# Performance work log

Hardware: AMD Instinct MI355X
Metric: run time of the kernel (lower is better)

The kernel has to match this reference:

```python
import jax, jax.numpy as jnp
import numpy as np

N, E, F, S = 20000, 160000, 16, 8
ECC1, ECC2, ECC3 = 40, 24, 24
DS = [96, 256, 768, 512, 64, 1]


def setup_inputs() -> dict:
    key = jax.random.key(0)
    ks = iter(jax.random.split(key, 40))
    inp = {}
    inp["x"] = jax.random.normal(next(ks), (N, F), dtype=jnp.float32)
    inp["edge_index"] = jax.random.randint(next(ks), (E, 2), 0, N, dtype=jnp.int32)
    inp["e"] = jax.random.uniform(next(ks), (E, S), dtype=jnp.float32)

    def dense_p(k, fi, fo):
        return (jax.random.normal(k, (fi, fo), dtype=jnp.float32) * (1.0 / np.sqrt(fi)),
                jnp.zeros((fo,), dtype=jnp.float32))

    # ECCConv params: kernel_network dense (S -> F_in*F_out), root kernel, bias
    for i, (fi, fo) in enumerate([(F, ECC1), (ECC1, ECC2), (ECC2, ECC3)], start=1):
        We, be = dense_p(next(ks), S, fi * fo)
        root, _ = dense_p(next(ks), fi, fo)
        inp[f"We{i}"], inp[f"be{i}"] = We, be
        inp[f"root{i}"], inp[f"b{i}"] = root, jnp.zeros((fo,), dtype=jnp.float32)

    dims = [ECC3] + DS
    for i in range(6):
        W, b = dense_p(next(ks), dims[i], dims[i + 1])
        inp[f"Wd{i+1}"], inp[f"bd{i+1}"] = W, b
    return inp


def _ecc(h, src, tgt, e, We, be, root, b):
    fi, fo = root.shape
    # per-edge filter matrices from edge features: [E, F_in, F_out]
    K = (e @ We + be).reshape(e.shape[0], fi, fo)
    msg = jnp.einsum('ef,efo->eo', h[src], K)          # gather + per-edge matvec
    agg = jax.ops.segment_sum(msg, tgt, num_segments=h.shape[0])  # scatter-add
    return jax.nn.relu(agg + h @ root + b)


def reference(x, edge_index, e,
              We1, be1, root1, b1,
              We2, be2, root2, b2,
              We3, be3, root3, b3,
              Wd1, bd1, Wd2, bd2, Wd3, bd3, Wd4, bd4, Wd5, bd5, Wd6, bd6):
    src, tgt = edge_index[:, 0], edge_index[:, 1]
    h = _ecc(x, src, tgt, e, We1, be1, root1, b1)
    h = _ecc(h, src, tgt, e, We2, be2, root2, b2)
    h = _ecc(h, src, tgt, e, We3, be3, root3, b3)
    g = jnp.sum(h, axis=0, keepdims=True)  # GlobalSumPool (single mode) -> [1, 24]
    for W, b in [(Wd1, bd1), (Wd2, bd2), (Wd3, bd3), (Wd4, bd4), (Wd5, bd5)]:
        g = jax.nn.relu(g @ W + b)
    return g @ Wd6 + bd6  # [1, 1]
```

## Files before the change

kernel.cpp:

```cpp
#include <hip/hip_runtime.h>

constexpr int NN  = 20000;
constexpr int NE  = 160000;
constexpr int CAP = 32;
constexpr int TN  = 32;
constexpr int NBM = 16;

__device__ inline void gstore(float* p, float v) {
    __hip_atomic_store(p, v, __ATOMIC_RELAXED, __HIP_MEMORY_SCOPE_AGENT);
}
__device__ inline float gload(const float* p) {
    return __hip_atomic_load(p, __ATOMIC_RELAXED, __HIP_MEMORY_SCOPE_AGENT);
}

__device__ inline void mbarrier(int* ctr, int target, bool wait) {
    __syncthreads();
    if (threadIdx.x == 0) {
        __threadfence();
        __hip_atomic_fetch_add(ctr, 1, __ATOMIC_ACQ_REL, __HIP_MEMORY_SCOPE_AGENT);
        if (wait)
            while (__hip_atomic_load(ctr, __ATOMIC_ACQUIRE, __HIP_MEMORY_SCOPE_AGENT) < target) {}
    }
    __syncthreads();
}

template<int FI, int FO2>
__device__ void stage_W(float* Wlds, const float* __restrict__ We,
                        const float* __restrict__ be, const float* __restrict__ root)
{
    constexpr int PW = 10 * FO2, C4 = PW / 4, O4 = FO2 / 4;
    for (int t = threadIdx.x; t < FI * C4; t += 256) {
        const int f = t / C4, r = t % C4, s = r / O4, oq = r % O4;
        const float4* src;
        if (s < 8)       src = (const float4*)(We + (size_t)s * FI * FO2 + f * FO2 + oq * 4);
        else if (s == 8) src = (const float4*)(be + f * FO2 + oq * 4);
        else             src = (const float4*)(root + f * FO2 + oq * 4);
        ((float4*)Wlds)[t] = *src;
    }
}

template<int FI, int FO2>
__device__ void gemm_tile(const float* htile, const float* Wlds,
                          const float* __restrict__ bias, float* __restrict__ Pout, int n0)
{
    constexpr int PW = 10 * FO2, C4 = PW / 4, O4 = FO2 / 4;
    constexpr int TPN = 256 / TN;
    const int nl = threadIdx.x / TPN;
    const int lane = threadIdx.x % TPN;
    const int n = n0 + nl;
    if (n >= NN) return;
    const float*  hr = &htile[nl * (FI + 4)];
    const float4* W4 = (const float4*)Wlds;
    float4* Pr = (float4*)(Pout + (size_t)n * PW);
    for (int cc = lane; cc < C4; cc += TPN) {
        float4 a = {0.f, 0.f, 0.f, 0.f};
        #pragma unroll
        for (int f = 0; f < FI; f++) {
            const float  hf = hr[f];
            const float4 w  = W4[f * C4 + cc];
            a.x = fmaf(hf, w.x, a.x); a.y = fmaf(hf, w.y, a.y);
            a.z = fmaf(hf, w.z, a.z); a.w = fmaf(hf, w.w, a.w);
        }
        if (cc >= 9 * O4) {
            const float4 b4 = ((const float4*)bias)[cc - 9 * O4];
            a.x += b4.x; a.y += b4.y; a.z += b4.z; a.w += b4.w;
        }
        Pr[cc] = a;
    }
}

__global__ __launch_bounds__(256)
void fill_nodeP1_kernel(const int* __restrict__ eidx, const float* __restrict__ x,
                        const float* __restrict__ We1, const float* __restrict__ be1,
                        const float* __restrict__ root1, const float* __restrict__ b1,
                        int* __restrict__ cnt_s, int* __restrict__ cnt_t,
                        int* __restrict__ se_eid, int* __restrict__ te_slot,
                        float* __restrict__ Pa)
{
    __shared__ float smem[16 * 400 + TN * 20];
    const int b = blockIdx.x, tid = threadIdx.x;
    if (b < 625) {
        const int eid = b * 256 + tid;
        const int2 st = ((const int2*)eidx)[eid];
        const int qs = atomicAdd(&cnt_s[st.x], 1);
        if (qs < CAP) {
            se_eid[st.x * CAP + qs] = eid;
            const int qt = atomicAdd(&cnt_t[st.y], 1);
            if (qt < CAP) te_slot[st.y * CAP + qt] = st.x * CAP + qs;
        }
    } else {
        float* Wlds  = smem;
        float* htile = smem + 6400;
        stage_W<16, 40>(Wlds, We1, be1, root1);
        const int n0 = (b - 625) * TN;
        for (int t = tid; t < TN * 4; t += 256) {
            const int nl = t / 4, fq = t % 4;
            const int n = n0 + nl;
            float4 v = {0.f, 0.f, 0.f, 0.f};
            if (n < NN) v = ((const float4*)(x + (size_t)n * 16))[fq];
            *((float4*)&htile[nl * 20 + fq * 4]) = v;
        }
        __syncthreads();
        gemm_tile<16, 40>(htile, Wlds, b1, Pa, n0);
    }
}

template<int FO, int PW1, int GSZ>
__global__ __launch_bounds__(256)
void push_msg_kernel(const float* __restrict__ Pin, const int* __restrict__ cnt_s,
                     const int* __restrict__ se_eid, const float* __restrict__ e,
                     float* __restrict__ msg)
{
    constexpr int SPB = 256 / GSZ;
    const int tid = threadIdx.x;
    const int o   = tid % GSZ;
    const int n   = blockIdx.x * SPB + tid / GSZ;

    float p[9];
    if (o < FO) {
        #pragma unroll
        for (int s = 0; s < 9; s++)
            p[s] = Pin[(size_t)n * PW1 + s * FO + o];
    }
    const int d = min(cnt_s[n], CAP);
    const int* eb = se_eid + n * CAP;
    float* mb = msg + (size_t)n * CAP * FO;
    #pragma unroll 2
    for (int j = 0; j < d; j++) {
        const int eid = eb[j];
        const float4 e0 = *(const float4*)(e + (size_t)eid * 8);
        const float4 e1 = *(const float4*)(e + (size_t)eid * 8 + 4);
        if (o < FO) {
            float m = p[8];
            m = fmaf(e0.x, p[0], m); m = fmaf(e0.y, p[1], m);
            m = fmaf(e0.z, p[2], m); m = fmaf(e0.w, p[3], m);
            m = fmaf(e1.x, p[4], m); m = fmaf(e1.y, p[5], m);
            m = fmaf(e1.z, p[6], m); m = fmaf(e1.w, p[7], m);
            mb[j * FO + o] = m;
        }
    }
}

template<int FI, int FO2>
__global__ __launch_bounds__(256)
void msg_gemm_kernel(const float* __restrict__ msg, const int* __restrict__ cnt_t,
                     const int* __restrict__ te_slot, const float* __restrict__ Pin,
                     const float* __restrict__ We, const float* __restrict__ be,
                     const float* __restrict__ root, const float* __restrict__ bias,
                     float* __restrict__ Pout)
{
    constexpr int PW_IN = 10 * FI, HS = FI + 4, OQ = FI / 4;
    __shared__ float smem[FI * 10 * FO2 + TN * HS];
    float* Wlds  = smem;
    float* htile = smem + FI * 10 * FO2;
    stage_W<FI, FO2>(Wlds, We, be, root);
    const int n0 = blockIdx.x * TN;
    for (int t = threadIdx.x; t < TN * OQ; t += 256) {
        const int nl = t / OQ, oq = t % OQ;
        const int n = n0 + nl;
        float4 acc = *(const float4*)(Pin + (size_t)n * PW_IN + 9 * FI + oq * 4);
        const int d = min(cnt_t[n], CAP);
        const int* tb = te_slot + n * CAP;
        #pragma unroll 2
        for (int k = 0; k < d; k++) {
            const int slot = tb[k];
            const float4 v = *(const float4*)(msg + (size_t)slot * FI + oq * 4);
            acc.x += v.x; acc.y += v.y; acc.z += v.z; acc.w += v.w;
        }
        float4 r = {fmaxf(acc.x, 0.f), fmaxf(acc.y, 0.f),
                    fmaxf(acc.z, 0.f), fmaxf(acc.w, 0.f)};
        *(float4*)&htile[nl * HS + oq * 4] = r;
    }
    __syncthreads();
    gemm_tile<FI, FO2>(htile, Wlds, bias, Pout, n0);
}

__global__ __launch_bounds__(256)
void msg_colsum_kernel(const float* __restrict__ msg, const int* __restrict__ cnt_t,
                       const int* __restrict__ te_slot, const float* __restrict__ Pin,
                       float* __restrict__ g)
{
    constexpr int FO = 24, OQ = 6;
    __shared__ float gl[FO];
    const int tid = threadIdx.x;
    if (tid < FO) gl[tid] = 0.f;
    __syncthreads();
    for (int i = blockIdx.x * 256 + tid; i < NN * OQ; i += gridDim.x * 256) {
        const int n = i / OQ, oq = i - n * OQ;
        float4 acc = *(const float4*)(Pin + (size_t)n * 240 + 216 + oq * 4);
        const int d = min(cnt_t[n], CAP);
        const int* tb = te_slot + n * CAP;
        #pragma unroll 2
        for (int k = 0; k < d; k++) {
            const int slot = tb[k];
            const float4 v = *(const float4*)(msg + (size_t)slot * FO + oq * 4);
            acc.x += v.x; acc.y += v.y; acc.z += v.z; acc.w += v.w;
        }
        atomicAdd(&gl[oq * 4 + 0], fmaxf(acc.x, 0.f));
        atomicAdd(&gl[oq * 4 + 1], fmaxf(acc.y, 0.f));
        atomicAdd(&gl[oq * 4 + 2], fmaxf(acc.z, 0.f));
        atomicAdd(&gl[oq * 4 + 3], fmaxf(acc.w, 0.f));
    }
    __syncthreads();
    if (tid < FO) unsafeAtomicAdd(&g[tid], gl[tid]);
}

__global__ __launch_bounds__(256)
void mlp_kernel(const float* __restrict__ g, int* __restrict__ ctr,
                const float* __restrict__ Wd1, const float* __restrict__ bd1,
                const float* __restrict__ Wd2, const float* __restrict__ bd2,
                const float* __restrict__ Wd3, const float* __restrict__ bd3,
                const float* __restrict__ Wd4, const float* __restrict__ bd4,
                const float* __restrict__ Wd5, const float* __restrict__ bd5,
                const float* __restrict__ Wd6, const float* __restrict__ bd6,
                float* __restrict__ m3, float* __restrict__ m4,
                float* __restrict__ out)
{
    __shared__ float v0[768];
    __shared__ float v1[96];
    __shared__ float red[256];
    const int tid = threadIdx.x, b = blockIdx.x;

    if (tid < 24) v0[tid] = g[tid];
    __syncthreads();
    if (tid < 96) {
        float a = bd1[tid];
        #pragma unroll
        for (int i = 0; i < 24; i++) a = fmaf(v0[i], Wd1[i * 96 + tid], a);
        v1[tid] = fmaxf(a, 0.f);
    }
    __syncthreads();

    {
        float a = bd2[tid];
        #pragma unroll
        for (int i = 0; i < 96; i++) a = fmaf(v1[i], Wd2[i * 256 + tid], a);
        red[tid] = fmaxf(a, 0.f);
    }
    __syncthreads();
    v0[tid] = red[tid];
    __syncthreads();

    if (tid < 192) {
        const int o = b * 48 + (tid % 48), kg = tid / 48;
        float a = 0.f;
        #pragma unroll 8
        for (int i = kg * 64; i < kg * 64 + 64; i++)
            a = fmaf(v0[i], Wd3[(size_t)i * 768 + o], a);
        red[tid] = a;
    }
    __syncthreads();
    if (tid < 48) {
        float s = bd3[b * 48 + tid] + red[tid] + red[48 + tid] + red[96 + tid] + red[144 + tid];
        gstore(&m3[b * 48 + tid], fmaxf(s, 0.f));
    }
    mbarrier(ctr, 1 * NBM, true);

    for (int i = tid; i < 768; i += 256) v0[i] = gload(&m3[i]);
    __syncthreads();
    {
        const int o = b * 32 + (tid & 31), kg = tid >> 5;
        float a = 0.f;
        #pragma unroll 8
        for (int i = kg * 96; i < kg * 96 + 96; i++)
            a = fmaf(v0[i], Wd4[(size_t)i * 512 + o], a);
        red[tid] = a;
    }
    __syncthreads();
    if (tid < 32) {
        float s = bd4[b * 32 + tid];
        #pragma unroll
        for (int k = 0; k < 8; k++) s += red[k * 32 + tid];
        gstore(&m4[b * 32 + tid], fmaxf(s, 0.f));
    }
    mbarrier(ctr, 2 * NBM, b == 0);

    if (b == 0) {
        for (int i = tid; i < 512; i += 256) v0[i] = gload(&m4[i]);
        __syncthreads();
        {
            const int o = tid & 63, kg = tid >> 6;
            float a = 0.f;
            #pragma unroll 8
            for (int i = kg * 128; i < kg * 128 + 128; i++)
                a = fmaf(v0[i], Wd5[(size_t)i * 64 + o], a);
            red[tid] = a;
        }
        __syncthreads();
        if (tid < 64) {
            float s = bd5[tid] + red[tid] + red[64 + tid] + red[128 + tid] + red[192 + tid];
            float v = fmaxf(s, 0.f) * Wd6[tid];
            #pragma unroll
            for (int off = 32; off > 0; off >>= 1)
                v += __shfl_down(v, off, 64);
            if (tid == 0) out[0] = v + bd6[0];
        }
    }
}

extern "C" void kernel_launch(void* const* d_in, const int* in_sizes, int n_in,
                              void* d_out, int out_size, void* d_ws, size_t ws_size,
                              hipStream_t stream)
{
    const float* x     = (const float*)d_in[0];
    const int*   eidx  = (const int*)  d_in[1];
    const float* e     = (const float*)d_in[2];
    const float* We1   = (const float*)d_in[3];  const float* be1 = (const float*)d_in[4];
    const float* root1 = (const float*)d_in[5];  const float* b1  = (const float*)d_in[6];
    const float* We2   = (const float*)d_in[7];  const float* be2 = (const float*)d_in[8];
    const float* root2 = (const float*)d_in[9];  const float* b2  = (const float*)d_in[10];
    const float* We3   = (const float*)d_in[11]; const float* be3 = (const float*)d_in[12];
    const float* root3 = (const float*)d_in[13]; const float* b3  = (const float*)d_in[14];
    const float* Wd1 = (const float*)d_in[15]; const float* bd1 = (const float*)d_in[16];
    const float* Wd2 = (const float*)d_in[17]; const float* bd2 = (const float*)d_in[18];
    const float* Wd3 = (const float*)d_in[19]; const float* bd3 = (const float*)d_in[20];
    const float* Wd4 = (const float*)d_in[21]; const float* bd4 = (const float*)d_in[22];
    const float* Wd5 = (const float*)d_in[23]; const float* bd5 = (const float*)d_in[24];
    const float* Wd6 = (const float*)d_in[25]; const float* bd6 = (const float*)d_in[26];

    int*   wi      = (int*)d_ws;
    float* wf      = (float*)d_ws;
    int*   cnt_s   = wi;
    int*   cnt_t   = wi + 20000;
    float* g       = wf + 40000;
    int*   mctr    = wi + 40064;
    float* m3      = wf + 40096;
    float* m4      = m3 + 768;
    int*   se_eid  = wi + 41376;
    int*   te_slot = wi + 681376;
    float* Pa      = wf + 1321376;
    float* Pb      = wf + 9321376;
    float* msg     = wf + 14121376;

    hipMemsetAsync(d_ws, 0, (size_t)41376 * sizeof(float), stream);

    fill_nodeP1_kernel<<<1250, 256, 0, stream>>>(eidx, x, We1, be1, root1, b1,
                                                 cnt_s, cnt_t, se_eid, te_slot, Pa);

    push_msg_kernel<40, 400, 64><<<NN / 4, 256, 0, stream>>>(Pa, cnt_s, se_eid, e, msg);

    msg_gemm_kernel<40, 24><<<625, 256, 0, stream>>>(msg, cnt_t, te_slot, Pa,
                                                     We2, be2, root2, b2, Pb);

    push_msg_kernel<24, 240, 32><<<NN / 8, 256, 0, stream>>>(Pb, cnt_s, se_eid, e, msg);

    msg_gemm_kernel<24, 24><<<625, 256, 0, stream>>>(msg, cnt_t, te_slot, Pb,
                                                     We3, be3, root3, b3, Pa);

    push_msg_kernel<24, 240, 32><<<NN / 8, 256, 0, stream>>>(Pa, cnt_s, se_eid, e, msg);

    msg_colsum_kernel<<<512, 256, 0, stream>>>(msg, cnt_t, te_slot, Pa, g);

    mlp_kernel<<<NBM, 256, 0, stream>>>(g, mctr,
                                        Wd1, bd1, Wd2, bd2, Wd3, bd3,
                                        Wd4, bd4, Wd5, bd5, Wd6, bd6,
                                        m3, m4, (float*)d_out);
}
```

Before: 263.1 us.

## Fuse per-layer node GEMM with edge message push, keep P tile in LDS

Merges each layer's node GEMM with the following edge-message push kernel, so the per-node 9-segment projection stays in LDS and only the root/bias segment is written to global memory. Tiles shrink to 8 nodes per block, weights are staged in two halves to fit LDS, and the target-side gather is split across several threads per feature with LDS atomics. Bucketing moves into its own kernel. This removes the large global P round-trip and two launches, but it restages the full weight matrix in every one of 2500 blocks and adds more barriers.

Result: no change. 258.3 us (-1.8%).

```diff
diff --git a/kernel.cpp b/kernel.cpp
--- a/kernel.cpp
+++ b/kernel.cpp
@@ -3,7 +3,7 @@
 constexpr int NN  = 20000;
 constexpr int NE  = 160000;
 constexpr int CAP = 32;
-constexpr int TN  = 32;
+constexpr int TN2 = 8;
 constexpr int NBM = 16;
 
 __device__ inline void gstore(float* p, float v) {
@@ -24,160 +24,225 @@
     __syncthreads();
 }
 
-template<int FI, int FO2>
-__device__ void stage_W(float* Wlds, const float* __restrict__ We,
-                        const float* __restrict__ be, const float* __restrict__ root)
-{
-    constexpr int PW = 10 * FO2, C4 = PW / 4, O4 = FO2 / 4;
-    for (int t = threadIdx.x; t < FI * C4; t += 256) {
-        const int f = t / C4, r = t % C4, s = r / O4, oq = r % O4;
+template<int FI, int FO2, int CH>
+__device__ void stage_half(float* Wh, const float* __restrict__ We,
+                           const float* __restrict__ be, const float* __restrict__ root,
+                           int c0)
+{
+    constexpr int O4 = FO2 / 4;
+    for (int t = threadIdx.x; t < FI * CH; t += 256) {
+        const int f = t / CH, ccp = t % CH, cc = c0 + ccp;
+        const int s = cc / O4, oq = cc % O4;
         const float4* src;
         if (s < 8)       src = (const float4*)(We + (size_t)s * FI * FO2 + f * FO2 + oq * 4);
         else if (s == 8) src = (const float4*)(be + f * FO2 + oq * 4);
         else             src = (const float4*)(root + f * FO2 + oq * 4);
-        ((float4*)Wlds)[t] = *src;
+        ((float4*)Wh)[t] = *src;
     }
 }
 
 template<int FI, int FO2>
-__device__ void gemm_tile(const float* htile, const float* Wlds,
-                          const float* __restrict__ bias, float* __restrict__ Pout, int n0)
-{
-    constexpr int PW = 10 * FO2, C4 = PW / 4, O4 = FO2 / 4;
-    constexpr int TPN = 256 / TN;
-    const int nl = threadIdx.x / TPN;
-    const int lane = threadIdx.x % TPN;
-    const int n = n0 + nl;
-    if (n >= NN) return;
-    const float*  hr = &htile[nl * (FI + 4)];
-    const float4* W4 = (const float4*)Wlds;
-    float4* Pr = (float4*)(Pout + (size_t)n * PW);
-    for (int cc = lane; cc < C4; cc += TPN) {
+__device__ void gemm_half_PL(const float* htile, const float* Wh,
+                             const float* __restrict__ bias,
+                             float* P_lds, float* __restrict__ seg9g,
+                             int n0, int c0)
+{
+    constexpr int PW = 10 * FO2, C4 = PW / 4, CH = C4 / 2, O4 = FO2 / 4;
+    constexpr int PL = 9 * FO2;
+    constexpr int TPN = 256 / TN2;
+    constexpr int HS  = FI + 4;
+    const int nl = threadIdx.x / TPN, lane = threadIdx.x % TPN;
+    const float*  hr = &htile[nl * HS];
+    const float4* W4 = (const float4*)Wh;
+    for (int ccp = lane; ccp < CH; ccp += TPN) {
+        const int cc = c0 + ccp;
         float4 a = {0.f, 0.f, 0.f, 0.f};
         #pragma unroll
         for (int f = 0; f < FI; f++) {
             const float  hf = hr[f];
-            const float4 w  = W4[f * C4 + cc];
+            const float4 w  = W4[f * CH + ccp];
             a.x = fmaf(hf, w.x, a.x); a.y = fmaf(hf, w.y, a.y);
             a.z = fmaf(hf, w.z, a.z); a.w = fmaf(hf, w.w, a.w);
         }
-        if (cc >= 9 * O4) {
+        if (cc < 9 * O4) {
+            *(float4*)&P_lds[nl * PL + cc * 4] = a;
+        } else {
             const float4 b4 = ((const float4*)bias)[cc - 9 * O4];
             a.x += b4.x; a.y += b4.y; a.z += b4.z; a.w += b4.w;
-        }
-        Pr[cc] = a;
+            *(float4*)&seg9g[(size_t)(n0 + nl) * FO2 + (cc - 9 * O4) * 4] = a;
+        }
+    }
+}
+
+template<int FO2>
+__device__ void push_phase(const float* P_lds, const int* __restrict__ cnt_s,
+                           const int* __restrict__ se_eid, const float* __restrict__ e,
+                           float* __restrict__ msg, float* scratch, int n0)
+{
+    constexpr int PL = 9 * FO2, OQ2 = FO2 / 4;
+    float* elds = scratch;
+    int*   esl  = (int*)(scratch + 2048);
+    int*   enl  = esl + 256;
+    int*   offs = enl + 256;
+    const int tid = threadIdx.x;
+    if (tid == 0) {
+        int a = 0;
+        for (int i = 0; i < TN2; i++) { offs[i] = a; a += min(cnt_s[n0 + i], CAP); }
+        offs[TN2] = a;
+    }
+    __syncthreads();
+    const int ET = offs[TN2];
+    for (int T = tid; T < ET; T += 256) {
+        int nl = 0;
+        #pragma unroll
+        for (int i = 1; i < TN2; i++) nl += (T >= offs[i]);
+        const int j    = T - offs[nl];
+        const int slot = (n0 + nl) * CAP + j;
+        const int eid  = se_eid[slot];
+        esl[T] = slot; enl[T] = nl;
+        *(float4*)&elds[T * 8]     = *(const float4*)(e + (size_t)eid * 8);
+        *(float4*)&elds[T * 8 + 4] = *(const float4*)(e + (size_t)eid * 8 + 4);
+    }
+    __syncthreads();
+    for (int T = tid; T < ET * OQ2; T += 256) {
+        const int ed = T / OQ2, oq = T % OQ2;
+        const int nl = enl[ed], slot = esl[ed];
+        const float* Pr = &P_lds[nl * PL + oq * 4];
+        const float* ee = &elds[ed * 8];
+        float4 m = *(const float4*)(Pr + 8 * FO2);
+        #pragma unroll
+        for (int s = 0; s < 8; s++) {
+            const float  es = ee[s];
+            const float4 w  = *(const float4*)(Pr + s * FO2);
+            m.x = fmaf(es, w.x, m.x); m.y = fmaf(es, w.y, m.y);
+            m.z = fmaf(es, w.z, m.z); m.w = fmaf(es, w.w, m.w);
+        }
+        *(float4*)&msg[(size_t)slot * FO2 + oq * 4] = m;
     }
 }
 
 __global__ __launch_bounds__(256)
-void fill_nodeP1_kernel(const int* __restrict__ eidx, const float* __restrict__ x,
-                        const float* __restrict__ We1, const float* __restrict__ be1,
-                        const float* __restrict__ root1, const float* __restrict__ b1,
-                        int* __restrict__ cnt_s, int* __restrict__ cnt_t,
-                        int* __restrict__ se_eid, int* __restrict__ te_slot,
-                        float* __restrict__ Pa)
-{
-    __shared__ float smem[16 * 400 + TN * 20];
-    const int b = blockIdx.x, tid = threadIdx.x;
-    if (b < 625) {
-        const int eid = b * 256 + tid;
-        const int2 st = ((const int2*)eidx)[eid];
-        const int qs = atomicAdd(&cnt_s[st.x], 1);
-        if (qs < CAP) {
-            se_eid[st.x * CAP + qs] = eid;
-            const int qt = atomicAdd(&cnt_t[st.y], 1);
-            if (qt < CAP) te_slot[st.y * CAP + qt] = st.x * CAP + qs;
-        }
-    } else {
-        float* Wlds  = smem;
-        float* htile = smem + 6400;
-        stage_W<16, 40>(Wlds, We1, be1, root1);
-        const int n0 = (b - 625) * TN;
-        for (int t = tid; t < TN * 4; t += 256) {
-            const int nl = t / 4, fq = t % 4;
-            const int n = n0 + nl;
-            float4 v = {0.f, 0.f, 0.f, 0.f};
-            if (n < NN) v = ((const float4*)(x + (size_t)n * 16))[fq];
-            *((float4*)&htile[nl * 20 + fq * 4]) = v;
-        }
-        __syncthreads();
-        gemm_tile<16, 40>(htile, Wlds, b1, Pa, n0);
-    }
-}
-
-template<int FO, int PW1, int GSZ>
-__global__ __launch_bounds__(256)
-void push_msg_kernel(const float* __restrict__ Pin, const int* __restrict__ cnt_s,
-                     const int* __restrict__ se_eid, const float* __restrict__ e,
-                     float* __restrict__ msg)
-{
-    constexpr int SPB = 256 / GSZ;
+void bucket_kernel(const int* __restrict__ eidx,
+                   int* __restrict__ cnt_s, int* __restrict__ cnt_t,
+                   int* __restrict__ se_eid, int* __restrict__ te_slot)
+{
+    const int eid = blockIdx.x * 256 + threadIdx.x;
+    const int2 st = ((const int2*)eidx)[eid];
+    const int qs = atomicAdd(&cnt_s[st.x], 1);
+    if (qs < CAP) {
+        se_eid[st.x * CAP + qs] = eid;
+        const int qt = atomicAdd(&cnt_t[st.y], 1);
+        if (qt < CAP) te_slot[st.y * CAP + qt] = st.x * CAP + qs;
+    }
+}
+
+__global__ __launch_bounds__(256, 4)
+void l1_push_kernel(const float* __restrict__ x,
+                    const float* __restrict__ We1, const float* __restrict__ be1,
+                    const float* __restrict__ root1, const float* __restrict__ b1,
+                    const int* __restrict__ cnt_s, const int* __restrict__ se_eid,
+                    const float* __restrict__ e,
+                    float* __restrict__ seg9_1, float* __restrict__ msg1)
+{
+    constexpr int FI = 16, FO2 = 40, CH = 50;
+    constexpr int WHF = FI * CH * 4;
+    constexpr int PLF = TN2 * 9 * FO2;
+    constexpr int HTF = TN2 * (FI + 4);
+    __shared__ float smem[WHF + PLF + HTF];
+    float* Wh    = smem;
+    float* P_lds = smem + WHF;
+    float* htile = smem + WHF + PLF;
     const int tid = threadIdx.x;
-    const int o   = tid % GSZ;
-    const int n   = blockIdx.x * SPB + tid / GSZ;
-
-    float p[9];
-    if (o < FO) {
-        #pragma unroll
-        for (int s = 0; s < 9; s++)
-            p[s] = Pin[(size_t)n * PW1 + s * FO + o];
-    }
-    const int d = min(cnt_s[n], CAP);
-    const int* eb = se_eid + n * CAP;
-    float* mb = msg + (size_t)n * CAP * FO;
-    #pragma unroll 2
-    for (int j = 0; j < d; j++) {
-        const int eid = eb[j];
-        const float4 e0 = *(const float4*)(e + (size_t)eid * 8);
-        const float4 e1 = *(const float4*)(e + (size_t)eid * 8 + 4);
-        if (o < FO) {
-            float m = p[8];
-            m = fmaf(e0.x, p[0], m); m = fmaf(e0.y, p[1], m);
-            m = fmaf(e0.z, p[2], m); m = fmaf(e0.w, p[3], m);
-            m = fmaf(e1.x, p[4], m); m = fmaf(e1.y, p[5], m);
-            m = fmaf(e1.z, p[6], m); m = fmaf(e1.w, p[7], m);
-            mb[j * FO + o] = m;
-        }
-    }
-}
-
-template<int FI, int FO2>
-__global__ __launch_bounds__(256)
-void msg_gemm_kernel(const float* __restrict__ msg, const int* __restrict__ cnt_t,
-                     const int* __restrict__ te_slot, const float* __restrict__ Pin,
-                     const float* __restrict__ We, const float* __restrict__ be,
-                     const float* __restrict__ root, const float* __restrict__ bias,
-                     float* __restrict__ Pout)
-{
-    constexpr int PW_IN = 10 * FI, HS = FI + 4, OQ = FI / 4;
-    __shared__ float smem[FI * 10 * FO2 + TN * HS];
-    float* Wlds  = smem;
-    float* htile = smem + FI * 10 * FO2;
-    stage_W<FI, FO2>(Wlds, We, be, root);
-    const int n0 = blockIdx.x * TN;
-    for (int t = threadIdx.x; t < TN * OQ; t += 256) {
-        const int nl = t / OQ, oq = t % OQ;
+    const int n0  = blockIdx.x * TN2;
+
+    stage_half<FI, FO2, CH>(Wh, We1, be1, root1, 0);
+    for (int t = tid; t < TN2 * 4; t += 256) {
+        const int nl = t / 4, fq = t % 4;
+        *(float4*)&htile[nl * 20 + fq * 4] =
+            *(const float4*)(x + (size_t)(n0 + nl) * 16 + fq * 4);
+    }
+    __syncthreads();
+    gemm_half_PL<FI, FO2>(htile, Wh, b1, P_lds, seg9_1, n0, 0);
+    __syncthreads();
+    stage_half<FI, FO2, CH>(Wh, We1, be1, root1, CH);
+    __syncthreads();
+    gemm_half_PL<FI, FO2>(htile, Wh, b1, P_lds, seg9_1, n0, CH);
+    __syncthreads();
+    push_phase<FO2>(P_lds, cnt_s, se_eid, e, msg1, Wh, n0);
+}
+
+template<int FI, int FO2, int J>
+__global__ __launch_bounds__(256, 4)
+void gather_gemm_push_kernel(const float* __restrict__ msg_prev,
+                             const int* __restrict__ cnt_t, const int* __restrict__ te_slot,
+                             const float* __restrict__ seg9_prev,
+                             const float* __restrict__ We, const float* __restrict__ be,
+                             const float* __restrict__ root, const float* __restrict__ bias,
+                             const int* __restrict__ cnt_s, const int* __restrict__ se_eid,
+                             const float* __restrict__ e,
+                             float* __restrict__ seg9_next, float* __restrict__ msg_next)
+{
+    constexpr int CH  = (10 * FO2 / 4) / 2;
+    constexpr int OQi = FI / 4;
+    constexpr int HS  = FI + 4;
+    constexpr int WHF = FI * CH * 4;
+    constexpr int PLF = TN2 * 9 * FO2;
+    constexpr int HTF = TN2 * HS;
+    __shared__ float smem[WHF + PLF + HTF];
+    float* Wh    = smem;
+    float* P_lds = smem + WHF;
+    float* htile = smem + WHF + PLF;
+    const int tid = threadIdx.x;
+    const int n0  = blockIdx.x * TN2;
+
+    stage_half<FI, FO2, CH>(Wh, We, be, root, 0);
+    for (int t = tid; t < TN2 * OQi; t += 256) {
+        const int nl = t / OQi, oq = t % OQi;
+        *(float4*)&htile[nl * HS + oq * 4] =
+            *(const float4*)(seg9_prev + (size_t)(n0 + nl) * FI + oq * 4);
+    }
+    __syncthreads();
+
+    for (int T = tid; T < TN2 * OQi * J; T += 256) {
+        const int nl = T / (OQi * J), r = T % (OQi * J), oq = r / J, jh = r % J;
         const int n = n0 + nl;
-        float4 acc = *(const float4*)(Pin + (size_t)n * PW_IN + 9 * FI + oq * 4);
         const int d = min(cnt_t[n], CAP);
+        if (jh >= d) continue;
+        float4 acc = {0.f, 0.f, 0.f, 0.f};
         const int* tb = te_slot + n * CAP;
-        #pragma unroll 2
-        for (int k = 0; k < d; k++) {
+        for (int k = jh; k < d; k += J) {
             const int slot = tb[k];
-            const float4 v = *(const float4*)(msg + (size_t)slot * FI + oq * 4);
+            const float4 v = *(const float4*)(msg_prev + (size_t)slot * FI + oq * 4);
             acc.x += v.x; acc.y += v.y; acc.z += v.z; acc.w += v.w;
         }
-        float4 r = {fmaxf(acc.x, 0.f), fmaxf(acc.y, 0.f),
-                    fmaxf(acc.z, 0.f), fmaxf(acc.w, 0.f)};
-        *(float4*)&htile[nl * HS + oq * 4] = r;
-    }
-    __syncthreads();
-    gemm_tile<FI, FO2>(htile, Wlds, bias, Pout, n0);
+        float* hp = &htile[nl * HS + oq * 4];
+        atomicAdd(hp + 0, acc.x);
+        atomicAdd(hp + 1, acc.y);
+        atomicAdd(hp + 2, acc.z);
+        atomicAdd(hp + 3, acc.w);
+    }
+    __syncthreads();
+    for (int t = tid; t < TN2 * OQi; t += 256) {
+        float4* p = (float4*)&htile[(t / OQi) * HS + (t % OQi) * 4];
+        float4 v = *p;
+        v.x = fmaxf(v.x, 0.f); v.y = fmaxf(v.y, 0.f);
+        v.z = fmaxf(v.z, 0.f); v.w = fmaxf(v.w, 0.f);
+        *p = v;
+    }
+    __syncthreads();
+
+    gemm_half_PL<FI, FO2>(htile, Wh, bias, P_lds, seg9_next, n0, 0);
+    __syncthreads();
+    stage_half<FI, FO2, CH>(Wh, We, be, root, CH);
+    __syncthreads();
+    gemm_half_PL<FI, FO2>(htile, Wh, bias, P_lds, seg9_next, n0, CH);
+    __syncthreads();
+    push_phase<FO2>(P_lds, cnt_s, se_eid, e, msg_next, Wh, n0);
 }
 
 __global__ __launch_bounds__(256)
 void msg_colsum_kernel(const float* __restrict__ msg, const int* __restrict__ cnt_t,
-                       const int* __restrict__ te_slot, const float* __restrict__ Pin,
+                       const int* __restrict__ te_slot, const float* __restrict__ seg9,
                        float* __restrict__ g)
 {
     constexpr int FO = 24, OQ = 6;
@@ -187,7 +252,7 @@
     __syncthreads();
     for (int i = blockIdx.x * 256 + tid; i < NN * OQ; i += gridDim.x * 256) {
         const int n = i / OQ, oq = i - n * OQ;
-        float4 acc = *(const float4*)(Pin + (size_t)n * 240 + 216 + oq * 4);
+        float4 acc = *(const float4*)(seg9 + (size_t)n * FO + oq * 4);
         const int d = min(cnt_t[n], CAP);
         const int* tb = te_slot + n * CAP;
         #pragma unroll 2
@@ -230,7 +295,6 @@
         v1[tid] = fmaxf(a, 0.f);
     }
     __syncthreads();
-
     {
         float a = bd2[tid];
         #pragma unroll
@@ -328,28 +392,29 @@
     float* m4      = m3 + 768;
     int*   se_eid  = wi + 41376;
     int*   te_slot = wi + 681376;
-    float* Pa      = wf + 1321376;
-    float* Pb      = wf + 9321376;
-    float* msg     = wf + 14121376;
+    float* seg9_1  = wf + 1321376;
+    float* seg9_2  = wf + 2121376;
+    float* seg9_3  = wf + 2601376;
+    float* msg1    = wf + 3081376;
+    float* msg3    = msg1;
+    float* msg2    = wf + 28681376;
 
     hipMemsetAsync(d_ws, 0, (size_t)41376 * sizeof(float), stream);
 
-    fill_nodeP1_kernel<<<1250, 256, 0, stream>>>(eidx, x, We1, be1, root1, b1,
-                                                 cnt_s, cnt_t, se_eid, te_slot, Pa);
-
-    push_msg_kernel<40, 400, 64><<<NN / 4, 256, 0, stream>>>(Pa, cnt_s, se_eid, e, msg);
-
-    msg_gemm_kernel<40, 24><<<625, 256, 0, stream>>>(msg, cnt_t, te_slot, Pa,
-                                                     We2, be2, root2, b2, Pb);
-
-    push_msg_kernel<24, 240, 32><<<NN / 8, 256, 0, stream>>>(Pb, cnt_s, se_eid, e, msg);
-
-    msg_gemm_kernel<24, 24><<<625, 256, 0, stream>>>(msg, cnt_t, te_slot, Pb,
-                                                     We3, be3, root3, b3, Pa);
-
-    push_msg_kernel<24, 240, 32><<<NN / 8, 256, 0, stream>>>(Pa, cnt_s, se_eid, e, msg);
-
-    msg_colsum_kernel<<<512, 256, 0, stream>>>(msg, cnt_t, te_slot, Pa, g);
+    bucket_kernel<<<625, 256, 0, stream>>>(eidx, cnt_s, cnt_t, se_eid, te_slot);
+
+    l1_push_kernel<<<NN / TN2, 256, 0, stream>>>(x, We1, be1, root1, b1,
+                                                 cnt_s, se_eid, e, seg9_1, msg1);
+
+    gather_gemm_push_kernel<40, 24, 3><<<NN / TN2, 256, 0, stream>>>(
+        msg1, cnt_t, te_slot, seg9_1, We2, be2, root2, b2,
+        cnt_s, se_eid, e, seg9_2, msg2);
+
+    gather_gemm_push_kernel<24, 24, 5><<<NN / TN2, 256, 0, stream>>>(
+        msg2, cnt_t, te_slot, seg9_2, We3, be3, root3, b3,
+        cnt_s, se_eid, e, seg9_3, msg3);
+
+    msg_colsum_kernel<<<512, 256, 0, stream>>>(msg3, cnt_t, te_slot, seg9_3, g);
 
     mlp_kernel<<<NBM, 256, 0, stream>>>(g, mctr,
                                         Wd1, bd1, Wd2, bd2, Wd3, bd3,
```
